# Kernel optimization log

Measured on AMD Instinct MI355X. Metric: run time of the kernel, lower is better.

Reference implementation:

```python
import jax, jax.numpy as jnp
import numpy as np

B, N, D = 8, 1024, 512
H = 8
DH = D // H
EPS_DIST = 1e-8
EPS_LN = 1e-5


def _layer_norm(x, gamma, beta):
    mu = jnp.mean(x, axis=-1, keepdims=True)
    var = jnp.mean((x - mu) ** 2, axis=-1, keepdims=True)
    return (x - mu) * jax.lax.rsqrt(var + EPS_LN) * gamma + beta


def setup_inputs() -> dict:
    key = jax.random.key(0)
    ks = jax.random.split(key, 6)
    scale = 1.0 / np.sqrt(D)
    inp = {
        "x": jax.random.normal(ks[0], (B, N, D), dtype=jnp.float32),
        "Wq": jax.random.normal(ks[1], (D, D), dtype=jnp.float32) * scale,
        "Wk": jax.random.normal(ks[2], (D, D), dtype=jnp.float32) * scale,
        "Wv": jax.random.normal(ks[3], (D, D), dtype=jnp.float32) * scale,
        "Wo": jax.random.normal(ks[4], (D, D), dtype=jnp.float32) * scale,
        "bq": jnp.zeros((D,), jnp.float32),
        "bk": jnp.zeros((D,), jnp.float32),
        "bv": jnp.zeros((D,), jnp.float32),
        "bo": jnp.zeros((D,), jnp.float32),
        "ln1_g": jnp.ones((D,), jnp.float32),
        "ln1_b": jnp.zeros((D,), jnp.float32),
        "ln2_g": jnp.ones((D,), jnp.float32),
        "ln2_b": jnp.zeros((D,), jnp.float32),
    }
    return inp


def reference(x, Wq, bq, Wk, bk, Wv, bv, Wo, bo, ln1_g, ln1_b, ln2_g, ln2_b):
    residual = x
    h = _layer_norm(x, ln1_g, ln1_b)  # pre-norm

    def heads(t):
        # [B,N,D] -> [B,H,N,DH]
        return t.reshape(B, N, H, DH).transpose(0, 2, 1, 3)

    q = heads(h @ Wq + bq)
    k = heads(h @ Wk + bk)
    v = heads(h @ Wv + bv)

    # Euclidean pairwise distance via ||q||^2 + ||k||^2 - 2 q.k expansion
    q_sq = jnp.sum(q * q, axis=-1)[..., :, None]      # [B,H,N,1]
    k_sq = jnp.sum(k * k, axis=-1)[..., None, :]      # [B,H,1,N]
    qk = jnp.einsum("bhnd,bhmd->bhnm", q, k)          # [B,H,N,N]
    d2 = jnp.maximum(q_sq + k_sq - 2.0 * qk, 0.0)
    dist = jnp.sqrt(d2 + EPS_DIST)

    # distance -> attention score: smaller distance = higher attention
    attn = jax.nn.softmax(-dist, axis=-1)             # [B,H,N,N]

    out = jnp.einsum("bhnm,bhmd->bhnd", attn, v)      # [B,H,N,DH]
    out = out.transpose(0, 2, 1, 3).reshape(B, N, D)
    out = out @ Wo + bo

    y = residual + out
    y = _layer_norm(y, ln2_g, ln2_b)
    return y
```

## Files before the change

### kernel.cpp

```cpp
#include <hip/hip_runtime.h>
#include <math.h>

typedef __attribute__((ext_vector_type(8))) short short8;
typedef __attribute__((ext_vector_type(4))) float f32x4;

constexpr int B  = 8;
constexpr int N  = 1024;
constexpr int D  = 512;
constexpr int H  = 8;
constexpr int DH = 64;
constexpr int M_ROWS = 8192;
constexpr float EPS_DIST = 1e-8f;
constexpr float EPS_LN   = 1e-5f;

__device__ inline unsigned short bfbits(float f) {
    union { float f; unsigned u; } v; v.f = f;
    unsigned r = v.u + 0x7fffu + ((v.u >> 16) & 1u);
    return (unsigned short)(r >> 16);
}
__device__ inline float bf2f(unsigned short s) {
    union { unsigned u; float f; } v; v.u = ((unsigned)s) << 16; return v.f;
}

__device__ inline void async_ld16(unsigned short* lds, const unsigned short* g) {
    __builtin_amdgcn_global_load_lds(
        (const __attribute__((address_space(1))) unsigned int*)(g),
        (__attribute__((address_space(3))) unsigned int*)(lds),
        16, 0, 0);
}

__device__ inline float block_sum256(float s, float* red) {
    for (int o = 32; o > 0; o >>= 1) s += __shfl_down(s, o, 64);
    int lane = threadIdx.x & 63, wid = threadIdx.x >> 6;
    if (lane == 0) red[wid] = s;
    __syncthreads();
    if (threadIdx.x == 0) red[4] = red[0] + red[1] + red[2] + red[3];
    __syncthreads();
    return red[4];
}

__global__ __launch_bounds__(256) void prep_kernel(const float* __restrict__ Wq,
                                                   const float* __restrict__ Wk,
                                                   const float* __restrict__ Wv,
                                                   const float* __restrict__ Wo,
                                                   unsigned short* __restrict__ WtAll,
                                                   const float* __restrict__ x,
                                                   const float* __restrict__ ln1_g,
                                                   const float* __restrict__ ln1_b,
                                                   unsigned short* __restrict__ h_bf) {
    __shared__ float red[8];
    const int bxg = blockIdx.x;
    if (bxg < 256) {
        int sub = bxg >> 6;
        const float* W = sub == 0 ? Wq : sub == 1 ? Wk : sub == 2 ? Wv : Wo;
        unsigned short* Wt = WtAll + (size_t)sub * 262144;
        int t = (bxg & 63) * 256 + threadIdx.x;
        int tn = t & 127, tk = t >> 7;
        int k = tk * 4, n = tn * 4;
        float4 r0 = *(const float4*)&W[(size_t)(k + 0) * 512 + n];
        float4 r1 = *(const float4*)&W[(size_t)(k + 1) * 512 + n];
        float4 r2 = *(const float4*)&W[(size_t)(k + 2) * 512 + n];
        float4 r3 = *(const float4*)&W[(size_t)(k + 3) * 512 + n];
        ushort4 c;
        c.x = bfbits(r0.x); c.y = bfbits(r1.x); c.z = bfbits(r2.x); c.w = bfbits(r3.x);
        *(ushort4*)&Wt[(size_t)(n + 0) * 512 + k] = c;
        c.x = bfbits(r0.y); c.y = bfbits(r1.y); c.z = bfbits(r2.y); c.w = bfbits(r3.y);
        *(ushort4*)&Wt[(size_t)(n + 1) * 512 + k] = c;
        c.x = bfbits(r0.z); c.y = bfbits(r1.z); c.z = bfbits(r2.z); c.w = bfbits(r3.z);
        *(ushort4*)&Wt[(size_t)(n + 2) * 512 + k] = c;
        c.x = bfbits(r0.w); c.y = bfbits(r1.w); c.z = bfbits(r2.w); c.w = bfbits(r3.w);
        *(ushort4*)&Wt[(size_t)(n + 3) * 512 + k] = c;
    } else {
        const int row = bxg - 256;
        const int t = threadIdx.x;
        const float* xr = x + (size_t)row * D;
        float v0 = xr[t], v1 = xr[t + 256];
        float mu = block_sum256(v0 + v1, red) * (1.0f / D);
        float d0 = v0 - mu, d1 = v1 - mu;
        float var = block_sum256(d0 * d0 + d1 * d1, red) * (1.0f / D);
        float rstd = rsqrtf(var + EPS_LN);
        h_bf[(size_t)row * D + t]       = bfbits(d0 * rstd * ln1_g[t] + ln1_b[t]);
        h_bf[(size_t)row * D + t + 256] = bfbits(d1 * rstd * ln1_g[t + 256] + ln1_b[t + 256]);
    }
}

__global__ __launch_bounds__(256) void ln2_kernel(const unsigned short* __restrict__ y0,
                                                  const float* __restrict__ res,
                                                  const float* __restrict__ gamma,
                                                  const float* __restrict__ beta,
                                                  float* __restrict__ out) {
    __shared__ float red[8];
    const int row = blockIdx.x;
    const int t = threadIdx.x;
    const unsigned short* xr = y0 + (size_t)row * D;
    const float* rr = res + (size_t)row * D;
    float v0 = bf2f(xr[t]) + rr[t];
    float v1 = bf2f(xr[t + 256]) + rr[t + 256];
    float mu = block_sum256(v0 + v1, red) * (1.0f / D);
    float d0 = v0 - mu, d1 = v1 - mu;
    float var = block_sum256(d0 * d0 + d1 * d1, red) * (1.0f / D);
    float rstd = rsqrtf(var + EPS_LN);
    out[(size_t)row * D + t]       = d0 * rstd * gamma[t] + beta[t];
    out[(size_t)row * D + t + 256] = d1 * rstd * gamma[t + 256] + beta[t + 256];
}

template <int MT>
__global__ __launch_bounds__(256) void gemm_qkv(const unsigned short* __restrict__ A,
                                                const unsigned short* __restrict__ Wt,
                                                const float* __restrict__ bias0,
                                                const float* __restrict__ bias1,
                                                const float* __restrict__ bias2,
                                                unsigned short* __restrict__ Qo,
                                                unsigned short* __restrict__ Ko,
                                                unsigned short* __restrict__ Vo,
                                                float* __restrict__ sq0,
                                                float* __restrict__ sq1) {
    constexpr int RB = M_ROWS / MT;
    constexpr int NI = MT / 32;
    constexpr int ASZ = MT * 64, BSZ = 128 * 64;
    constexpr int SMSZ = (ASZ + BSZ > 18432) ? ASZ + BSZ : 18432;
    __shared__ unsigned short smem[SMSZ];
    unsigned short* As = smem;
    unsigned short* Bs = smem + ASZ;

    const int id = blockIdx.x;
    const int by = id & (RB - 1), bx = id / RB;
    const int tid = threadIdx.x;
    const int lane = tid & 63, wv = tid >> 6;
    const int quad = lane >> 4, l15 = lane & 15;
    const int row0 = by * MT, col0 = bx * 128;
    const int wm = (wv & 1) * (MT / 2), wn = (wv >> 1) * 64;

    f32x4 acc[NI][4];
    #pragma unroll
    for (int i = 0; i < NI; ++i)
        #pragma unroll
        for (int j = 0; j < 4; ++j) acc[i][j] = (f32x4){0.f, 0.f, 0.f, 0.f};

    const unsigned short* Ag = A  + (size_t)row0 * 512;
    const unsigned short* Bg = Wt + (size_t)col0 * 512;

    for (int k0 = 0; k0 < 512; k0 += 64) {
        __syncthreads();
        #pragma unroll
        for (int c = 0; c < ASZ / 2048; ++c) {
            int fu = c * 2048 + tid * 8;
            int r = fu >> 6, ko = fu & 63;
            async_ld16(As + fu, Ag + (size_t)r * 512 + k0 + ko);
        }
        #pragma unroll
        for (int c = 0; c < BSZ / 2048; ++c) {
            int fu = c * 2048 + tid * 8;
            int r = fu >> 6, ko = fu & 63;
            async_ld16(Bs + fu, Bg + (size_t)r * 512 + k0 + ko);
        }
        __syncthreads();

        #pragma unroll
        for (int ks = 0; ks < 2; ++ks) {
            short8 af[NI], bf[4];
            #pragma unroll
            for (int i = 0; i < NI; ++i)
                af[i] = *(const short8*)&As[(wm + i * 16 + l15) * 64 + ks * 32 + quad * 8];
            #pragma unroll
            for (int j = 0; j < 4; ++j)
                bf[j] = *(const short8*)&Bs[(wn + j * 16 + l15) * 64 + ks * 32 + quad * 8];
            #pragma unroll
            for (int i = 0; i < NI; ++i)
                #pragma unroll
                for (int j = 0; j < 4; ++j)
                    acc[i][j] = __builtin_amdgcn_mfma_f32_16x16x32_bf16(af[i], bf[j], acc[i][j], 0, 0, 0);
        }
    }

    const int colg = col0 + wn;
    const int seg = colg >> 9;
    const int hh = (colg & 511) >> 6;
    const float* bias = seg == 0 ? bias0 : seg == 1 ? bias1 : bias2;

    if (seg < 2) {
        unsigned short* dst = seg == 0 ? Qo : Ko;
        float* sq = seg == 0 ? sq0 : sq1;
        #pragma unroll
        for (int i = 0; i < NI; ++i) {
            const int m0 = row0 + wm + i * 16 + quad * 4;
            float ss[4] = {0.f, 0.f, 0.f, 0.f};
            #pragma unroll
            for (int j = 0; j < 4; ++j) {
                float bvj = bias[hh * 64 + j * 16 + l15];
                #pragma unroll
                for (int r = 0; r < 4; ++r) {
                    float v = acc[i][j][r] + bvj;
                    unsigned short ub = bfbits(v);
                    float vr = bf2f(ub);
                    ss[r] += vr * vr;
                    int m = m0 + r;
                    int b_ = m >> 10, n_ = m & 1023;
                    dst[((size_t)((b_ * 8 + hh) * 1024) + n_) * 64 + j * 16 + l15] = ub;
                }
            }
            #pragma unroll
            for (int r = 0; r < 4; ++r) {
                float s = ss[r];
                s += __shfl_xor(s, 1, 64);
                s += __shfl_xor(s, 2, 64);
                s += __shfl_xor(s, 4, 64);
                s += __shfl_xor(s, 8, 64);
                if (l15 == 0) {
                    int m = m0 + r;
                    sq[(size_t)((m >> 10) * 8 + hh) * 1024 + (m & 1023)] = s;
                }
            }
        }
    } else {
        __syncthreads();
        unsigned short* T = smem + wv * 4608;
        #pragma unroll
        for (int i = 0; i < NI; ++i)
            #pragma unroll
            for (int j = 0; j < 4; ++j) {
                float bvj = bias[hh * 64 + j * 16 + l15];
                ushort4 pk;
                pk.x = bfbits(acc[i][j][0] + bvj);
                pk.y = bfbits(acc[i][j][1] + bvj);
                pk.z = bfbits(acc[i][j][2] + bvj);
                pk.w = bfbits(acc[i][j][3] + bvj);
                *(ushort4*)&T[(j * 16 + l15) * 72 + i * 16 + quad * 4] = pk;
            }
        const int b_ = (row0 + wm) >> 10;
        const int nbase = (row0 + wm) & 1023;
        unsigned short* Vg = Vo + ((size_t)((b_ * 8 + hh) * 64)) * 1024 + nbase;
        #pragma unroll
        for (int it = 0; it < 8; ++it) {
            int dl = it * 8 + (lane >> 3);
            int nl = (lane & 7) * 8;
            uint4 v = *(const uint4*)&T[dl * 72 + nl];
            *(uint4*)&Vg[(size_t)dl * 1024 + nl] = v;
        }
    }
}

__global__ __launch_bounds__(256) void gemm_out(const unsigned short* __restrict__ A,
                                                const unsigned short* __restrict__ Wt,
                                                const float* __restrict__ bias,
                                                unsigned short* __restrict__ C) {
    __shared__ unsigned short As[64 * 64];
    __shared__ unsigned short Bs[128 * 64];

    const int id = blockIdx.x;
    const int by = id & 127, bx = id >> 7;
    const int tid = threadIdx.x;
    const int lane = tid & 63, wv = tid >> 6;
    const int quad = lane >> 4, l15 = lane & 15;
    const int row0 = by * 64, col0 = bx * 128;
    const int wm = (wv & 1) * 32, wn = (wv >> 1) * 64;

    f32x4 acc[2][4];
    #pragma unroll
    for (int i = 0; i < 2; ++i)
        #pragma unroll
        for (int j = 0; j < 4; ++j) acc[i][j] = (f32x4){0.f, 0.f, 0.f, 0.f};

    const unsigned short* Ag = A  + (size_t)row0 * 512;
    const unsigned short* Bg = Wt + (size_t)col0 * 512;

    for (int k0 = 0; k0 < 512; k0 += 64) {
        __syncthreads();
        #pragma unroll
        for (int c = 0; c < 2; ++c) {
            int fu = c * 2048 + tid * 8;
            int r = fu >> 6, ko = fu & 63;
            async_ld16(As + fu, Ag + (size_t)r * 512 + k0 + ko);
        }
        #pragma unroll
        for (int c = 0; c < 4; ++c) {
            int fu = c * 2048 + tid * 8;
            int r = fu >> 6, ko = fu & 63;
            async_ld16(Bs + fu, Bg + (size_t)r * 512 + k0 + ko);
        }
        __syncthreads();

        #pragma unroll
        for (int ks = 0; ks < 2; ++ks) {
            short8 af[2], bf[4];
            #pragma unroll
            for (int i = 0; i < 2; ++i)
                af[i] = *(const short8*)&As[(wm + i * 16 + l15) * 64 + ks * 32 + quad * 8];
            #pragma unroll
            for (int j = 0; j < 4; ++j)
                bf[j] = *(const short8*)&Bs[(wn + j * 16 + l15) * 64 + ks * 32 + quad * 8];
            #pragma unroll
            for (int i = 0; i < 2; ++i)
                #pragma unroll
                for (int j = 0; j < 4; ++j)
                    acc[i][j] = __builtin_amdgcn_mfma_f32_16x16x32_bf16(af[i], bf[j], acc[i][j], 0, 0, 0);
        }
    }

    #pragma unroll
    for (int i = 0; i < 2; ++i)
        #pragma unroll
        for (int j = 0; j < 4; ++j) {
            int col = col0 + wn + j * 16 + l15;
            float bv = bias[col];
            #pragma unroll
            for (int r = 0; r < 4; ++r) {
                int row = row0 + wm + i * 16 + quad * 4 + r;
                C[(size_t)row * 512 + col] = bfbits(acc[i][j][r] + bv);
            }
        }
}

__global__ __launch_bounds__(256) void attn_kernel(const unsigned short* __restrict__ Q,
                                                   const unsigned short* __restrict__ K,
                                                   const unsigned short* __restrict__ Vt,
                                                   const float* __restrict__ qsq,
                                                   const float* __restrict__ ksq,
                                                   unsigned short* __restrict__ O) {
    __shared__ unsigned short Ks[64][72];
    __shared__ unsigned short Vs[64][72];
    __shared__ unsigned short Ps[4][16][72];
    __shared__ float ksq_s[64];

    const int id = blockIdx.x;
    const int bh = id & 63, qb = id >> 6;
    const int q0 = qb * 64;
    const int tid = threadIdx.x;
    const int lane = tid & 63, w = tid >> 6;
    const int quad = lane >> 4, l15 = lane & 15;
    const int b_ = bh >> 3, h_ = bh & 7;

    const unsigned short* Qb = Q  + (size_t)bh * N * DH;
    const unsigned short* Kb = K  + (size_t)bh * N * DH;
    const unsigned short* Vb = Vt + (size_t)bh * DH * N;

    short8 qf0, qf1;
    {
        const unsigned short* qp = Qb + (size_t)(q0 + w * 16 + l15) * 64 + quad * 8;
        qf0 = *(const short8*)qp;
        qf1 = *(const short8*)(qp + 32);
    }
    float qe[4];
    #pragma unroll
    for (int r = 0; r < 4; ++r)
        qe[r] = qsq[bh * N + q0 + w * 16 + quad * 4 + r] + EPS_DIST;

    f32x4 oacc[4];
    #pragma unroll
    for (int dt = 0; dt < 4; ++dt) oacc[dt] = (f32x4){0.f, 0.f, 0.f, 0.f};
    float dpart[4] = {};

    const int rr = tid >> 2, cc = (tid & 3) * 16;
    uint4 kreg0, kreg1, vreg0, vreg1;
    float ksreg = 0.f;

    kreg0 = *(const uint4*)(Kb + (size_t)rr * 64 + cc);
    kreg1 = *(const uint4*)(Kb + (size_t)rr * 64 + cc + 8);
    vreg0 = *(const uint4*)(Vb + (size_t)rr * N + cc);
    vreg1 = *(const uint4*)(Vb + (size_t)rr * N + cc + 8);
    if (tid < 64) ksreg = ksq[bh * N + tid];

    *(uint4*)&Ks[rr][cc]     = kreg0;
    *(uint4*)&Ks[rr][cc + 8] = kreg1;
    *(uint4*)&Vs[rr][cc]     = vreg0;
    *(uint4*)&Vs[rr][cc + 8] = vreg1;
    if (tid < 64) ksq_s[tid] = ksreg;
    __syncthreads();

    for (int kt = 0; kt < 16; ++kt) {
        if (kt < 15) {
            kreg0 = *(const uint4*)(Kb + (size_t)((kt + 1) * 64 + rr) * 64 + cc);
            kreg1 = *(const uint4*)(Kb + (size_t)((kt + 1) * 64 + rr) * 64 + cc + 8);
            vreg0 = *(const uint4*)(Vb + (size_t)rr * N + (kt + 1) * 64 + cc);
            vreg1 = *(const uint4*)(Vb + (size_t)rr * N + (kt + 1) * 64 + cc + 8);
            if (tid < 64) ksreg = ksq[bh * N + (kt + 1) * 64 + tid];
        }

        #pragma unroll
        for (int kb = 0; kb < 4; ++kb) {
            short8 kf0 = *(const short8*)&Ks[kb * 16 + l15][quad * 8];
            short8 kf1 = *(const short8*)&Ks[kb * 16 + l15][32 + quad * 8];
            float ks2 = ksq_s[kb * 16 + l15];
            f32x4 sa = (f32x4){0.f, 0.f, 0.f, 0.f};
            sa = __builtin_amdgcn_mfma_f32_16x16x32_bf16(qf0, kf0, sa, 0, 0, 0);
            sa = __builtin_amdgcn_mfma_f32_16x16x32_bf16(qf1, kf1, sa, 0, 0, 0);
            #pragma unroll
            for (int r = 0; r < 4; ++r) {
                float d2 = fmaf(-2.0f, sa[r], qe[r] + ks2);
                d2 = fmaxf(d2, EPS_DIST);
                float p = __expf(-__builtin_amdgcn_sqrtf(d2));
                dpart[r] += p;
                union { float f; unsigned u; } pu; pu.f = p;
                Ps[w][quad * 4 + r][kb * 16 + l15] = (unsigned short)(pu.u >> 16);
            }
        }

        short8 vf[4][2];
        #pragma unroll
        for (int dt = 0; dt < 4; ++dt)
            #pragma unroll
            for (int kc = 0; kc < 2; ++kc)
                vf[dt][kc] = *(const short8*)&Vs[dt * 16 + l15][kc * 32 + quad * 8];
        #pragma unroll
        for (int kc = 0; kc < 2; ++kc) {
            short8 pf = *(const short8*)&Ps[w][l15][kc * 32 + quad * 8];
            #pragma unroll
            for (int dt = 0; dt < 4; ++dt)
                oacc[dt] = __builtin_amdgcn_mfma_f32_16x16x32_bf16(pf, vf[dt][kc], oacc[dt], 0, 0, 0);
        }

        if (kt < 15) {
            __syncthreads();
            *(uint4*)&Ks[rr][cc]     = kreg0;
            *(uint4*)&Ks[rr][cc + 8] = kreg1;
            *(uint4*)&Vs[rr][cc]     = vreg0;
            *(uint4*)&Vs[rr][cc + 8] = vreg1;
            if (tid < 64) ksq_s[tid] = ksreg;
            __syncthreads();
        }
    }

    float rinv[4];
    #pragma unroll
    for (int r = 0; r < 4; ++r) {
        float s = dpart[r];
        s += __shfl_xor(s, 1, 64);
        s += __shfl_xor(s, 2, 64);
        s += __shfl_xor(s, 4, 64);
        s += __shfl_xor(s, 8, 64);
        rinv[r] = 1.0f / s;
    }

    #pragma unroll
    for (int dt = 0; dt < 4; ++dt)
        #pragma unroll
        for (int r = 0; r < 4; ++r) {
            int n_ = q0 + w * 16 + quad * 4 + r;
            O[((size_t)(b_ * N + n_) * D) + h_ * DH + dt * 16 + l15] =
                bfbits(oacc[dt][r] * rinv[r]);
        }
}

extern "C" void kernel_launch(void* const* d_in, const int* in_sizes, int n_in,
                              void* d_out, int out_size, void* d_ws, size_t ws_size,
                              hipStream_t stream) {
    const float* x     = (const float*)d_in[0];
    const float* Wq    = (const float*)d_in[1];
    const float* Wk    = (const float*)d_in[2];
    const float* Wv    = (const float*)d_in[3];
    const float* Wo    = (const float*)d_in[4];
    const float* bq    = (const float*)d_in[5];
    const float* bk    = (const float*)d_in[6];
    const float* bv    = (const float*)d_in[7];
    const float* bo    = (const float*)d_in[8];
    const float* ln1_g = (const float*)d_in[9];
    const float* ln1_b = (const float*)d_in[10];
    const float* ln2_g = (const float*)d_in[11];
    const float* ln2_b = (const float*)d_in[12];
    float* out = (float*)d_out;

    unsigned short* WtAll = (unsigned short*)d_ws;
    unsigned short* h_bf  = WtAll + 4 * 262144;
    unsigned short* Qb    = h_bf + 4194304;
    unsigned short* Kb    = Qb + 4194304;
    unsigned short* Vtg   = Kb + 4194304;
    unsigned short* Ob    = Vtg + 4194304;
    unsigned short* Y0    = Ob + 4194304;
    float* qsq = (float*)(Y0 + 4194304);
    float* ksq = qsq + 65536;

    prep_kernel<<<256 + M_ROWS, 256, 0, stream>>>(Wq, Wk, Wv, Wo, WtAll,
                                                  x, ln1_g, ln1_b, h_bf);

    gemm_qkv<128><<<768, 256, 0, stream>>>(h_bf, WtAll, bq, bk, bv,
                                           Qb, Kb, Vtg, qsq, ksq);

    attn_kernel<<<1024, 256, 0, stream>>>(Qb, Kb, Vtg, qsq, ksq, Ob);

    gemm_out<<<512, 256, 0, stream>>>(Ob, WtAll + 3 * 262144, bo, Y0);

    ln2_kernel<<<M_ROWS, 256, 0, stream>>>(Y0, x, ln2_g, ln2_b, out);
}
```

Baseline: 186.9 us.

## Use 32x32 MFMA tiles in attention and stage GEMM epilogues through LDS

The attention kernel now processes 128 queries per block (32 per wave) with 32x32x16 MFMA, computing S^T so each lane owns one query row. This halves the grid and raises K/V tile reuse per LDS load. The QKV and output GEMM epilogues now stage results in shared memory and write coalesced 16-byte stores instead of scattered 2-byte stores. The risks are the extra LDS traffic and syncs, and lower parallelism in attention from the smaller grid.

```diff
diff --git a/kernel.cpp b/kernel.cpp
--- a/kernel.cpp
+++ b/kernel.cpp
@@ -1,8 +1,9 @@
 #include <hip/hip_runtime.h>
 #include <math.h>
 
-typedef __attribute__((ext_vector_type(8))) short short8;
-typedef __attribute__((ext_vector_type(4))) float f32x4;
+typedef __attribute__((ext_vector_type(8)))  short short8;
+typedef __attribute__((ext_vector_type(4)))  float f32x4;
+typedef __attribute__((ext_vector_type(16))) float f32x16;
 
 constexpr int B  = 8;
 constexpr int N  = 1024;
@@ -178,6 +179,11 @@
     const int hh = (colg & 511) >> 6;
     const float* bias = seg == 0 ? bias0 : seg == 1 ? bias1 : bias2;
 
+    __syncthreads();
+    unsigned short* T = smem + wv * 4608;
+    const int b_ = (row0 + wm) >> 10;
+    const int nbase = (row0 + wm) & 1023;
+
     if (seg < 2) {
         unsigned short* dst = seg == 0 ? Qo : Ko;
         float* sq = seg == 0 ? sq0 : sq1;
@@ -194,9 +200,7 @@
                     unsigned short ub = bfbits(v);
                     float vr = bf2f(ub);
                     ss[r] += vr * vr;
-                    int m = m0 + r;
-                    int b_ = m >> 10, n_ = m & 1023;
-                    dst[((size_t)((b_ * 8 + hh) * 1024) + n_) * 64 + j * 16 + l15] = ub;
+                    T[(i * 16 + quad * 4 + r) * 72 + j * 16 + l15] = ub;
                 }
             }
             #pragma unroll
@@ -212,9 +216,14 @@
                 }
             }
         }
+        unsigned short* dg = dst + ((size_t)((b_ * 8 + hh) * 1024) + nbase) * 64;
+        #pragma unroll
+        for (int it = 0; it < 8; ++it) {
+            int rr2 = it * 8 + (lane >> 3);
+            int cc2 = (lane & 7) * 8;
+            *(uint4*)&dg[(size_t)rr2 * 64 + cc2] = *(const uint4*)&T[rr2 * 72 + cc2];
+        }
     } else {
-        __syncthreads();
-        unsigned short* T = smem + wv * 4608;
         #pragma unroll
         for (int i = 0; i < NI; ++i)
             #pragma unroll
@@ -227,8 +236,6 @@
                 pk.w = bfbits(acc[i][j][3] + bvj);
                 *(ushort4*)&T[(j * 16 + l15) * 72 + i * 16 + quad * 4] = pk;
             }
-        const int b_ = (row0 + wm) >> 10;
-        const int nbase = (row0 + wm) & 1023;
         unsigned short* Vg = Vo + ((size_t)((b_ * 8 + hh) * 64)) * 1024 + nbase;
         #pragma unroll
         for (int it = 0; it < 8; ++it) {
@@ -244,8 +251,9 @@
                                                 const unsigned short* __restrict__ Wt,
                                                 const float* __restrict__ bias,
                                                 unsigned short* __restrict__ C) {
-    __shared__ unsigned short As[64 * 64];
-    __shared__ unsigned short Bs[128 * 64];
+    __shared__ unsigned short smem[64 * 64 + 128 * 64];
+    unsigned short* As = smem;
+    unsigned short* Bs = smem + 64 * 64;
 
     const int id = blockIdx.x;
     const int by = id & 127, bx = id >> 7;
@@ -297,18 +305,24 @@
         }
     }
 
+    __syncthreads();
+    unsigned short* T = smem + wv * 2304;
     #pragma unroll
     for (int i = 0; i < 2; ++i)
         #pragma unroll
         for (int j = 0; j < 4; ++j) {
-            int col = col0 + wn + j * 16 + l15;
-            float bv = bias[col];
-            #pragma unroll
-            for (int r = 0; r < 4; ++r) {
-                int row = row0 + wm + i * 16 + quad * 4 + r;
-                C[(size_t)row * 512 + col] = bfbits(acc[i][j][r] + bv);
-            }
-        }
+            float bv = bias[col0 + wn + j * 16 + l15];
+            #pragma unroll
+            for (int r = 0; r < 4; ++r)
+                T[(i * 16 + quad * 4 + r) * 72 + j * 16 + l15] = bfbits(acc[i][j][r] + bv);
+        }
+    #pragma unroll
+    for (int it = 0; it < 4; ++it) {
+        int rr2 = it * 8 + (lane >> 3);
+        int cc2 = (lane & 7) * 8;
+        *(uint4*)&C[(size_t)(row0 + wm + rr2) * 512 + col0 + wn + cc2] =
+            *(const uint4*)&T[rr2 * 72 + cc2];
+    }
 }
 
 __global__ __launch_bounds__(256) void attn_kernel(const unsigned short* __restrict__ Q,
@@ -317,38 +331,40 @@
                                                    const float* __restrict__ qsq,
                                                    const float* __restrict__ ksq,
                                                    unsigned short* __restrict__ O) {
-    __shared__ unsigned short Ks[64][72];
-    __shared__ unsigned short Vs[64][72];
-    __shared__ unsigned short Ps[4][16][72];
+    __shared__ unsigned short Ks[64 * 72];
+    __shared__ unsigned short Vs[64 * 72];
+    __shared__ unsigned short Ps[4][32 * 72];
     __shared__ float ksq_s[64];
+    __shared__ float dinv_s[4][32];
 
     const int id = blockIdx.x;
     const int bh = id & 63, qb = id >> 6;
-    const int q0 = qb * 64;
+    const int q0 = qb * 128;
     const int tid = threadIdx.x;
     const int lane = tid & 63, w = tid >> 6;
-    const int quad = lane >> 4, l15 = lane & 15;
+    const int half = lane >> 5, l31 = lane & 31;
     const int b_ = bh >> 3, h_ = bh & 7;
 
     const unsigned short* Qb = Q  + (size_t)bh * N * DH;
     const unsigned short* Kb = K  + (size_t)bh * N * DH;
     const unsigned short* Vb = Vt + (size_t)bh * DH * N;
 
-    short8 qf0, qf1;
+    const int qrow = q0 + w * 32 + l31;
+
+    short8 qa[4];
     {
-        const unsigned short* qp = Qb + (size_t)(q0 + w * 16 + l15) * 64 + quad * 8;
-        qf0 = *(const short8*)qp;
-        qf1 = *(const short8*)(qp + 32);
-    }
-    float qe[4];
+        const unsigned short* qp = Qb + (size_t)qrow * 64 + half * 8;
+        #pragma unroll
+        for (int ks = 0; ks < 4; ++ks) qa[ks] = *(const short8*)(qp + ks * 16);
+    }
+    const float qeps = qsq[bh * N + qrow] + EPS_DIST;
+
+    f32x16 oacc[2];
     #pragma unroll
-    for (int r = 0; r < 4; ++r)
-        qe[r] = qsq[bh * N + q0 + w * 16 + quad * 4 + r] + EPS_DIST;
-
-    f32x4 oacc[4];
-    #pragma unroll
-    for (int dt = 0; dt < 4; ++dt) oacc[dt] = (f32x4){0.f, 0.f, 0.f, 0.f};
-    float dpart[4] = {};
+    for (int dt = 0; dt < 2; ++dt)
+        #pragma unroll
+        for (int r = 0; r < 16; ++r) oacc[dt][r] = 0.f;
+    float dpart = 0.f;
 
     const int rr = tid >> 2, cc = (tid & 3) * 16;
     uint4 kreg0, kreg1, vreg0, vreg1;
@@ -360,10 +376,10 @@
     vreg1 = *(const uint4*)(Vb + (size_t)rr * N + cc + 8);
     if (tid < 64) ksreg = ksq[bh * N + tid];
 
-    *(uint4*)&Ks[rr][cc]     = kreg0;
-    *(uint4*)&Ks[rr][cc + 8] = kreg1;
-    *(uint4*)&Vs[rr][cc]     = vreg0;
-    *(uint4*)&Vs[rr][cc + 8] = vreg1;
+    *(uint4*)&Ks[rr * 72 + cc]     = kreg0;
+    *(uint4*)&Ks[rr * 72 + cc + 8] = kreg1;
+    *(uint4*)&Vs[rr * 72 + cc]     = vreg0;
+    *(uint4*)&Vs[rr * 72 + cc + 8] = vreg1;
     if (tid < 64) ksq_s[tid] = ksreg;
     __syncthreads();
 
@@ -376,69 +392,76 @@
             if (tid < 64) ksreg = ksq[bh * N + (kt + 1) * 64 + tid];
         }
 
-        #pragma unroll
-        for (int kb = 0; kb < 4; ++kb) {
-            short8 kf0 = *(const short8*)&Ks[kb * 16 + l15][quad * 8];
-            short8 kf1 = *(const short8*)&Ks[kb * 16 + l15][32 + quad * 8];
-            float ks2 = ksq_s[kb * 16 + l15];
-            f32x4 sa = (f32x4){0.f, 0.f, 0.f, 0.f};
-            sa = __builtin_amdgcn_mfma_f32_16x16x32_bf16(qf0, kf0, sa, 0, 0, 0);
-            sa = __builtin_amdgcn_mfma_f32_16x16x32_bf16(qf1, kf1, sa, 0, 0, 0);
-            #pragma unroll
-            for (int r = 0; r < 4; ++r) {
-                float d2 = fmaf(-2.0f, sa[r], qe[r] + ks2);
-                d2 = fmaxf(d2, EPS_DIST);
-                float p = __expf(-__builtin_amdgcn_sqrtf(d2));
-                dpart[r] += p;
-                union { float f; unsigned u; } pu; pu.f = p;
-                Ps[w][quad * 4 + r][kb * 16 + l15] = (unsigned short)(pu.u >> 16);
+        f32x16 sacc[2];
+        #pragma unroll
+        for (int kb = 0; kb < 2; ++kb)
+            #pragma unroll
+            for (int r = 0; r < 16; ++r) sacc[kb][r] = 0.f;
+        #pragma unroll
+        for (int ks = 0; ks < 4; ++ks) {
+            short8 kf0 = *(const short8*)&Ks[(l31)      * 72 + ks * 16 + half * 8];
+            short8 kf1 = *(const short8*)&Ks[(32 + l31) * 72 + ks * 16 + half * 8];
+            sacc[0] = __builtin_amdgcn_mfma_f32_32x32x16_bf16(kf0, qa[ks], sacc[0], 0, 0, 0);
+            sacc[1] = __builtin_amdgcn_mfma_f32_32x32x16_bf16(kf1, qa[ks], sacc[1], 0, 0, 0);
+        }
+
+        #pragma unroll
+        for (int kb = 0; kb < 2; ++kb) {
+            #pragma unroll
+            for (int g = 0; g < 4; ++g) {
+                const int keyl = kb * 32 + 8 * g + 4 * half;
+                float4 ks2v = *(const float4*)&ksq_s[keyl];
+                union { float f; unsigned u; } p0, p1, p2, p3;
+                {
+                    float d2 = fmaf(-2.0f, sacc[kb][4 * g + 0], qeps + ks2v.x);
+                    p0.f = __expf(-__builtin_amdgcn_sqrtf(fmaxf(d2, EPS_DIST)));
+                    d2 = fmaf(-2.0f, sacc[kb][4 * g + 1], qeps + ks2v.y);
+                    p1.f = __expf(-__builtin_amdgcn_sqrtf(fmaxf(d2, EPS_DIST)));
+                    d2 = fmaf(-2.0f, sacc[kb][4 * g + 2], qeps + ks2v.z);
+                    p2.f = __expf(-__builtin_amdgcn_sqrtf(fmaxf(d2, EPS_DIST)));
+                    d2 = fmaf(-2.0f, sacc[kb][4 * g + 3], qeps + ks2v.w);
+                    p3.f = __expf(-__builtin_amdgcn_sqrtf(fmaxf(d2, EPS_DIST)));
+                }
+                dpart += (p0.f + p1.f) + (p2.f + p3.f);
+                uint2 pk;
+                pk.x = __builtin_amdgcn_perm(p1.u, p0.u, 0x07060302);
+                pk.y = __builtin_amdgcn_perm(p3.u, p2.u, 0x07060302);
+                *(uint2*)&Ps[w][l31 * 72 + keyl] = pk;
             }
         }
 
-        short8 vf[4][2];
-        #pragma unroll
-        for (int dt = 0; dt < 4; ++dt)
-            #pragma unroll
-            for (int kc = 0; kc < 2; ++kc)
-                vf[dt][kc] = *(const short8*)&Vs[dt * 16 + l15][kc * 32 + quad * 8];
-        #pragma unroll
-        for (int kc = 0; kc < 2; ++kc) {
-            short8 pf = *(const short8*)&Ps[w][l15][kc * 32 + quad * 8];
-            #pragma unroll
-            for (int dt = 0; dt < 4; ++dt)
-                oacc[dt] = __builtin_amdgcn_mfma_f32_16x16x32_bf16(pf, vf[dt][kc], oacc[dt], 0, 0, 0);
+        #pragma unroll
+        for (int ks = 0; ks < 4; ++ks) {
+            short8 pa  = *(const short8*)&Ps[w][l31 * 72 + ks * 16 + half * 8];
+            short8 vf0 = *(const short8*)&Vs[(l31)      * 72 + ks * 16 + half * 8];
+            short8 vf1 = *(const short8*)&Vs[(32 + l31) * 72 + ks * 16 + half * 8];
+            oacc[0] = __builtin_amdgcn_mfma_f32_32x32x16_bf16(pa, vf0, oacc[0], 0, 0, 0);
+            oacc[1] = __builtin_amdgcn_mfma_f32_32x32x16_bf16(pa, vf1, oacc[1], 0, 0, 0);
         }
 
         if (kt < 15) {
             __syncthreads();
-            *(uint4*)&Ks[rr][cc]     = kreg0;
-            *(uint4*)&Ks[rr][cc + 8] = kreg1;
-            *(uint4*)&Vs[rr][cc]     = vreg0;
-            *(uint4*)&Vs[rr][cc + 8] = vreg1;
+            *(uint4*)&Ks[rr * 72 + cc]     = kreg0;
+            *(uint4*)&Ks[rr * 72 + cc + 8] = kreg1;
+            *(uint4*)&Vs[rr * 72 + cc]     = vreg0;
+            *(uint4*)&Vs[rr * 72 + cc + 8] = vreg1;
             if (tid < 64) ksq_s[tid] = ksreg;
             __syncthreads();
         }
     }
 
-    float rinv[4];
+    dpart += __shfl_xor(dpart, 32, 64);
+    if (half == 0) dinv_s[w][l31] = 1.0f / dpart;
+
     #pragma unroll
-    for (int r = 0; r < 4; ++r) {
-        float s = dpart[r];
-        s += __shfl_xor(s, 1, 64);
-        s += __shfl_xor(s, 2, 64);
-        s += __shfl_xor(s, 4, 64);
-        s += __shfl_xor(s, 8, 64);
-        rinv[r] = 1.0f / s;
-    }
-
-    #pragma unroll
-    for (int dt = 0; dt < 4; ++dt)
-        #pragma unroll
-        for (int r = 0; r < 4; ++r) {
-            int n_ = q0 + w * 16 + quad * 4 + r;
-            O[((size_t)(b_ * N + n_) * D) + h_ * DH + dt * 16 + l15] =
-                bfbits(oacc[dt][r] * rinv[r]);
-        }
+    for (int r = 0; r < 16; ++r) {
+        const int lq = (r & 3) + 8 * (r >> 2) + 4 * half;
+        const float rinv = dinv_s[w][lq];
+        const int n_ = q0 + w * 32 + lq;
+        unsigned short* og = O + ((size_t)(b_ * N + n_) * D) + h_ * DH;
+        og[l31]      = bfbits(oacc[0][r] * rinv);
+        og[32 + l31] = bfbits(oacc[1][r] * rinv);
+    }
 }
 
 extern "C" void kernel_launch(void* const* d_in, const int* in_sizes, int n_in,
@@ -475,7 +498,7 @@
     gemm_qkv<128><<<768, 256, 0, stream>>>(h_bf, WtAll, bq, bk, bv,
                                            Qb, Kb, Vtg, qsq, ksq);
 
-    attn_kernel<<<1024, 256, 0, stream>>>(Qb, Kb, Vtg, qsq, ksq, Ob);
+    attn_kernel<<<512, 256, 0, stream>>>(Qb, Kb, Vtg, qsq, ksq, Ob);
 
     gemm_out<<<512, 256, 0, stream>>>(Ob, WtAll + 3 * 262144, bo, Y0);
 
```

Measured after the change: 185.1 us. No clear change (-0.9%).
